# Kernel tuning notes

Hardware: AMD Instinct MI355X
Metric: run time of the kernel (lower is better)

The kernel has to match this reference:

```python
import jax, jax.numpy as jnp
import numpy as np

N_NODES = 100000
HID = 64
IN_DIM = 128


def setup_inputs() -> dict:
    key = jax.random.key(0)
    ks = jax.random.split(key, 12)
    x = jax.random.normal(ks[0], (N_NODES, IN_DIM), dtype=jnp.float32)
    edge_index = jax.random.randint(ks[1], (2, 1600000), 0, N_NODES, dtype=jnp.int64)
    batch = jnp.zeros((N_NODES,), dtype=jnp.int64)
    def glorot(k, shape):
        fan_in, fan_out = shape
        lim = (6.0 / (fan_in + fan_out)) ** 0.5
        return jax.random.uniform(k, shape, jnp.float32, -lim, lim)
    return {
        "x": x,
        "edge_index": edge_index,
        "batch": batch,
        "W1": glorot(ks[2], (IN_DIM, HID)), "b1": jnp.zeros((HID,), jnp.float32),
        "W2": glorot(ks[3], (HID, HID)),   "b2": jnp.zeros((HID,), jnp.float32),
        "W3": glorot(ks[4], (HID, HID)),   "b3": jnp.zeros((HID,), jnp.float32),
        "Wp1": glorot(ks[5], (HID, HID // 2)), "bp1": jnp.zeros((HID // 2,), jnp.float32),
        "Wp2": glorot(ks[6], (HID // 2, 1)),   "bp2": jnp.zeros((1,), jnp.float32),
    }


def _gcn_norm(edge_index, n_nodes):
    # Add self-loops, compute symmetric normalization deg^{-1/2}[src]*deg^{-1/2}[dst]
    loops = jnp.arange(n_nodes, dtype=edge_index.dtype)
    src = jnp.concatenate([edge_index[0], loops])
    dst = jnp.concatenate([edge_index[1], loops])
    deg = jax.ops.segment_sum(jnp.ones_like(dst, dtype=jnp.float32), dst,
                              num_segments=n_nodes)
    dinv = jnp.where(deg > 0, jax.lax.rsqrt(deg), 0.0)
    norm = dinv[src] * dinv[dst]  # [E + N]
    return src, dst, norm


def _gcn_layer(x, src, dst, norm, W, b, n_nodes):
    h = x @ W                       # [N, out]  dense transform first (PyG order)
    msg = h[src] * norm[:, None]    # gather + scale, [E+N, out]
    agg = jax.ops.segment_sum(msg, dst, num_segments=n_nodes)  # scatter-add
    return agg + b


def reference(x, edge_index, batch, W1, b1, W2, b2, W3, b3, Wp1, bp1, Wp2, bp2):
    n = x.shape[0]
    src, dst, norm = _gcn_norm(edge_index, n)
    # eval mode: dropout is identity
    h = jax.nn.relu(_gcn_layer(x, src, dst, norm, W1, b1, n))
    h = jax.nn.relu(_gcn_layer(h, src, dst, norm, W2, b2, n))
    h = jax.nn.relu(_gcn_layer(h, src, dst, norm, W3, b3, n))
    h = jax.nn.relu(h @ Wp1 + bp1)
    return h @ Wp2 + bp2  # [N, 1] node predictions
```

## Files before the change

### kernel.cpp

```cpp
#include <hip/hip_runtime.h>
#include <hip/hip_bf16.h>
#include <hip/hip_fp16.h>

#define NDIM_IN 128
#define HID 64

#define BINW 128
#define NB   782
#define NC   256
#define CAP  3072

typedef _Float16 f16x8 __attribute__((ext_vector_type(8)));
typedef float f32x4 __attribute__((ext_vector_type(4)));

__global__ __launch_bounds__(256) void hist_k(const int* __restrict__ dst,
                                              int* __restrict__ histT, int E) {
  __shared__ int h[NB];
  for (int i = threadIdx.x; i < NB; i += 256) h[i] = 0;
  __syncthreads();
  int E4 = E >> 2;
  int chunk = (E4 + NC - 1) / NC;
  int beg = blockIdx.x * chunk;
  int end = min(E4, beg + chunk);
  const int4* __restrict__ d4 = (const int4*)dst;
  for (int i = beg + (int)threadIdx.x; i < end; i += 256) {
    int4 d = d4[i];
    atomicAdd(&h[d.x >> 7], 1);
    atomicAdd(&h[d.y >> 7], 1);
    atomicAdd(&h[d.z >> 7], 1);
    atomicAdd(&h[d.w >> 7], 1);
  }
  __syncthreads();
  for (int i = threadIdx.x; i < NB; i += 256)
    histT[i * NC + blockIdx.x] = h[i];
}

__global__ __launch_bounds__(256) void scan1(int* __restrict__ g,
                                             int* __restrict__ bs, int len) {
  __shared__ int s[256];
  int t = threadIdx.x;
  int i = blockIdx.x * 256 + t;
  int v = (i < len) ? g[i] : 0;
  s[t] = v;
  __syncthreads();
  for (int off = 1; off < 256; off <<= 1) {
    int x = (t >= off) ? s[t - off] : 0;
    __syncthreads();
    s[t] += x;
    __syncthreads();
  }
  if (i < len) g[i] = s[t] - v;
  if (t == 255) bs[blockIdx.x] = s[255];
}

__global__ __launch_bounds__(1024) void scan2(int* __restrict__ bs, int nb) {
  __shared__ int s[1024];
  int t = threadIdx.x;
  int v = (t < nb) ? bs[t] : 0;
  s[t] = v;
  __syncthreads();
  for (int off = 1; off < 1024; off <<= 1) {
    int x = (t >= off) ? s[t - off] : 0;
    __syncthreads();
    s[t] += x;
    __syncthreads();
  }
  if (t < nb) bs[t] = s[t] - v;
}

__global__ __launch_bounds__(256) void scatter_k(const int* __restrict__ src,
                                                 const int* __restrict__ dst,
                                                 const int* __restrict__ S,
                                                 const int* __restrict__ bsum,
                                                 int* __restrict__ tmp, int E) {
  __shared__ int cur[NB];
  for (int i = threadIdx.x; i < NB; i += 256)
    cur[i] = S[i * NC + blockIdx.x] + bsum[i];
  __syncthreads();
  int E4 = E >> 2;
  int chunk = (E4 + NC - 1) / NC;
  int beg = blockIdx.x * chunk;
  int end = min(E4, beg + chunk);
  const int4* __restrict__ d4 = (const int4*)dst;
  const int4* __restrict__ s4 = (const int4*)src;
  for (int i = beg + (int)threadIdx.x; i < end; i += 256) {
    int4 d = d4[i];
    int4 sv = s4[i];
    int p0 = atomicAdd(&cur[d.x >> 7], 1); tmp[p0] = (sv.x << 7) | (d.x & 127);
    int p1 = atomicAdd(&cur[d.y >> 7], 1); tmp[p1] = (sv.y << 7) | (d.y & 127);
    int p2 = atomicAdd(&cur[d.z >> 7], 1); tmp[p2] = (sv.z << 7) | (d.z & 127);
    int p3 = atomicAdd(&cur[d.w >> 7], 1); tmp[p3] = (sv.w << 7) | (d.w & 127);
  }
}

__global__ __launch_bounds__(256) void binsort_k(const int* __restrict__ tmp,
                                                 const int* __restrict__ bsum,
                                                 int* __restrict__ col,
                                                 int* __restrict__ rp,
                                                 float* __restrict__ dinv,
                                                 int n, int E) {
  int bin = blockIdx.x;
  int base = bsum[bin];
  int end = (bin == NB - 1) ? E : bsum[bin + 1];
  int m = end - base;
  __shared__ int cnt[BINW];
  __shared__ int offs[BINW];
  __shared__ int cur[BINW];
  __shared__ int buf[CAP];
  int t = threadIdx.x;
  if (t < BINW) cnt[t] = 0;
  __syncthreads();
  for (int i = t; i < m; i += 256) {
    int p = tmp[base + i];
    atomicAdd(&cnt[p & (BINW - 1)], 1);
  }
  __syncthreads();
  if (t < BINW) offs[t] = cnt[t];
  __syncthreads();
  for (int off = 1; off < BINW; off <<= 1) {
    int x = (t < BINW && t >= off) ? offs[t - off] : 0;
    __syncthreads();
    if (t < BINW) offs[t] += x;
    __syncthreads();
  }
  if (t < BINW) {
    int ex = offs[t] - cnt[t];
    cur[t] = ex;
    int v = bin * BINW + t;
    if (v < n) {
      rp[v] = base + ex;
      dinv[v] = rsqrtf((float)cnt[t] + 1.0f);
    }
  }
  if (bin == NB - 1 && t == 0) rp[n] = E;
  __syncthreads();
  for (int i = t; i < m; i += 256) {
    int p = tmp[base + i];
    int r = atomicAdd(&cur[p & (BINW - 1)], 1);
    if (r < CAP) buf[r] = p >> 7;
  }
  __syncthreads();
  int mm = min(m, CAP);
  for (int i = t; i < mm; i += 256) col[base + i] = buf[i];
}

template <int K>
__global__ __launch_bounds__(256) void gemm_mfma(const float* __restrict__ X,
                                                 const float* __restrict__ W,
                                                 const float* __restrict__ dinv,
                                                 __half* __restrict__ T,
                                                 int n, int ntiles) {
  constexpr int NCH = K / 32;
  __shared__ float Ds[4][16 * 68];
  int wv = threadIdx.x >> 6;
  int lane = threadIdx.x & 63;
  int colx = lane & 15;
  int quad = lane >> 4;

  f16x8 bf[4][NCH];
#pragma unroll
  for (int t = 0; t < 4; t++)
#pragma unroll
    for (int c = 0; c < NCH; c++) {
      f16x8 b;
#pragma unroll
      for (int j = 0; j < 8; j++)
        b[j] = (_Float16)W[(32 * c + quad * 8 + j) * 64 + 16 * t + colx];
      bf[t][c] = b;
    }

  for (int tile = blockIdx.x * 4 + wv; tile < ntiles; tile += gridDim.x * 4) {
    int node0 = tile * 16;
    f32x4 acc[4] = {{0.f, 0.f, 0.f, 0.f}, {0.f, 0.f, 0.f, 0.f},
                    {0.f, 0.f, 0.f, 0.f}, {0.f, 0.f, 0.f, 0.f}};
    int arow = min(node0 + colx, n - 1);
    const float* __restrict__ xr = X + (size_t)arow * K;
#pragma unroll
    for (int c = 0; c < NCH; c++) {
      float4 x0 = *(const float4*)(xr + 32 * c + quad * 8);
      float4 x1 = *(const float4*)(xr + 32 * c + quad * 8 + 4);
      f16x8 a;
      a[0] = (_Float16)x0.x; a[1] = (_Float16)x0.y;
      a[2] = (_Float16)x0.z; a[3] = (_Float16)x0.w;
      a[4] = (_Float16)x1.x; a[5] = (_Float16)x1.y;
      a[6] = (_Float16)x1.z; a[7] = (_Float16)x1.w;
#pragma unroll
      for (int t = 0; t < 4; t++)
        acc[t] = __builtin_amdgcn_mfma_f32_16x16x32_f16(a, bf[t][c], acc[t], 0, 0, 0);
    }
    float dv[4];
#pragma unroll
    for (int r = 0; r < 4; r++) {
      int nd = min(node0 + quad * 4 + r, n - 1);
      dv[r] = dinv[nd];
    }
#pragma unroll
    for (int t = 0; t < 4; t++)
#pragma unroll
      for (int r = 0; r < 4; r++)
        Ds[wv][(quad * 4 + r) * 68 + 16 * t + colx] = acc[t][r] * dv[r];
    int nd = node0 + colx;
    const float* __restrict__ row = &Ds[wv][colx * 68 + quad * 16];
    float4 y0 = *(const float4*)(row + 0);
    float4 y1 = *(const float4*)(row + 4);
    float4 y2 = *(const float4*)(row + 8);
    float4 y3 = *(const float4*)(row + 12);
    f16x8 o0, o1;
    o0[0] = (_Float16)y0.x; o0[1] = (_Float16)y0.y;
    o0[2] = (_Float16)y0.z; o0[3] = (_Float16)y0.w;
    o0[4] = (_Float16)y1.x; o0[5] = (_Float16)y1.y;
    o0[6] = (_Float16)y1.z; o0[7] = (_Float16)y1.w;
    o1[0] = (_Float16)y2.x; o1[1] = (_Float16)y2.y;
    o1[2] = (_Float16)y2.z; o1[3] = (_Float16)y2.w;
    o1[4] = (_Float16)y3.x; o1[5] = (_Float16)y3.y;
    o1[6] = (_Float16)y3.z; o1[7] = (_Float16)y3.w;
    if (nd < n) {
      uint4* __restrict__ o = (uint4*)(T + (size_t)nd * 64 + quad * 16);
      o[0] = *(uint4*)&o0;
      o[1] = *(uint4*)&o1;
    }
  }
}

__global__ __launch_bounds__(256) void spmm_relu(const int* __restrict__ rp,
                                                 const int* __restrict__ col,
                                                 const __half* __restrict__ T,
                                                 const float* __restrict__ dinv,
                                                 const float* __restrict__ bias,
                                                 float* __restrict__ H, int n) {
  int gid = blockIdx.x * 256 + threadIdx.x;
  int v = gid >> 6;
  int lane = gid & 63;
  if (v >= n) return;
  int g = lane >> 3;
  int sub = lane & 7;
  const uint4* __restrict__ T8 = (const uint4*)T;
  int beg = rp[v], end = rp[v + 1];

  float a0[8], a1[8];
#pragma unroll
  for (int j = 0; j < 8; j++) { a0[j] = 0.f; a1[j] = 0.f; }

  if (g == 0) {
    uint4 w = T8[v * 8 + sub];
    const __half2* h = (const __half2*)&w;
#pragma unroll
    for (int j = 0; j < 4; j++) {
      float2 f = __half22float2(h[j]);
      a0[2 * j] += f.x; a0[2 * j + 1] += f.y;
    }
  }
  int efull = beg + ((end - beg) & ~15);
  for (int e = beg; e < efull; e += 16) {
    int s0 = col[e + g];
    int s1 = col[e + 8 + g];
    uint4 w0 = T8[s0 * 8 + sub];
    uint4 w1 = T8[s1 * 8 + sub];
    const __half2* h0 = (const __half2*)&w0;
    const __half2* h1 = (const __half2*)&w1;
#pragma unroll
    for (int j = 0; j < 4; j++) {
      float2 f0 = __half22float2(h0[j]);
      float2 f1 = __half22float2(h1[j]);
      a0[2 * j] += f0.x; a0[2 * j + 1] += f0.y;
      a1[2 * j] += f1.x; a1[2 * j + 1] += f1.y;
    }
  }
  {
    int i0 = efull + g, i1 = efull + 8 + g;
    if (i0 < end) {
      uint4 w = T8[col[i0] * 8 + sub];
      const __half2* h = (const __half2*)&w;
#pragma unroll
      for (int j = 0; j < 4; j++) {
        float2 f = __half22float2(h[j]);
        a0[2 * j] += f.x; a0[2 * j + 1] += f.y;
      }
    }
    if (i1 < end) {
      uint4 w = T8[col[i1] * 8 + sub];
      const __half2* h = (const __half2*)&w;
#pragma unroll
      for (int j = 0; j < 4; j++) {
        float2 f = __half22float2(h[j]);
        a1[2 * j] += f.x; a1[2 * j + 1] += f.y;
      }
    }
  }
  float s[8];
#pragma unroll
  for (int j = 0; j < 8; j++) s[j] = a0[j] + a1[j];
#pragma unroll
  for (int j = 0; j < 8; j++) s[j] += __shfl_xor(s[j], 8);
#pragma unroll
  for (int j = 0; j < 8; j++) s[j] += __shfl_xor(s[j], 16);
#pragma unroll
  for (int j = 0; j < 8; j++) s[j] += __shfl_xor(s[j], 32);
  if (lane < 8) {
    float di = dinv[v];
    const float4* __restrict__ b4 = (const float4*)bias;
    float4 bA = b4[sub * 2], bB = b4[sub * 2 + 1];
    float4 rA, rB;
    rA.x = di * s[0] + bA.x; rA.y = di * s[1] + bA.y;
    rA.z = di * s[2] + bA.z; rA.w = di * s[3] + bA.w;
    rB.x = di * s[4] + bB.x; rB.y = di * s[5] + bB.y;
    rB.z = di * s[6] + bB.z; rB.w = di * s[7] + bB.w;
    rA.x = rA.x > 0.f ? rA.x : 0.f;  rA.y = rA.y > 0.f ? rA.y : 0.f;
    rA.z = rA.z > 0.f ? rA.z : 0.f;  rA.w = rA.w > 0.f ? rA.w : 0.f;
    rB.x = rB.x > 0.f ? rB.x : 0.f;  rB.y = rB.y > 0.f ? rB.y : 0.f;
    rB.z = rB.z > 0.f ? rB.z : 0.f;  rB.w = rB.w > 0.f ? rB.w : 0.f;
    float4* __restrict__ o = (float4*)(H + (size_t)v * HID + sub * 8);
    o[0] = rA;
    o[1] = rB;
  }
}

__global__ __launch_bounds__(256) void mlp_head(const float* __restrict__ H,
                                                const float* __restrict__ Wp1,
                                                const float* __restrict__ bp1,
                                                const float* __restrict__ Wp2,
                                                const float* __restrict__ bp2,
                                                float* __restrict__ out, int n) {
  __shared__ float W1t[32 * 64];
  __shared__ float w2s[32];
  __shared__ float b1s[32];
  for (int i = threadIdx.x; i < 64 * 32; i += 256) {
    int k = i >> 5, j = i & 31;
    W1t[j * 64 + k] = Wp1[i];
  }
  if (threadIdx.x < 32) {
    w2s[threadIdx.x] = Wp2[threadIdx.x];
    b1s[threadIdx.x] = bp1[threadIdx.x];
  }
  __syncthreads();
  int node = blockIdx.x * 256 + threadIdx.x;
  if (node >= n) return;
  float4 h[16];
  const float4* __restrict__ hr = (const float4*)(H + (size_t)node * 64);
#pragma unroll
  for (int j = 0; j < 16; j++) h[j] = hr[j];
  float o = bp2[0];
#pragma unroll
  for (int j = 0; j < 32; j++) {
    const float4* wr = (const float4*)(W1t + j * 64);
    float4 a4 = make_float4(0.f, 0.f, 0.f, 0.f);
#pragma unroll
    for (int k = 0; k < 16; k++) {
      float4 w = wr[k];
      a4.x += h[k].x * w.x;
      a4.y += h[k].y * w.y;
      a4.z += h[k].z * w.z;
      a4.w += h[k].w * w.w;
    }
    float a = a4.x + a4.y + a4.z + a4.w + b1s[j];
    a = a > 0.f ? a : 0.f;
    o += a * w2s[j];
  }
  out[node] = o;
}

extern "C" void kernel_launch(void* const* d_in, const int* in_sizes, int n_in,
                              void* d_out, int out_size, void* d_ws, size_t ws_size,
                              hipStream_t stream) {
  const float* x   = (const float*)d_in[0];
  const int* edge  = (const int*)d_in[1];
  const float* W1  = (const float*)d_in[3];
  const float* b1  = (const float*)d_in[4];
  const float* W2  = (const float*)d_in[5];
  const float* b2  = (const float*)d_in[6];
  const float* W3  = (const float*)d_in[7];
  const float* b3  = (const float*)d_in[8];
  const float* Wp1 = (const float*)d_in[9];
  const float* bp1 = (const float*)d_in[10];
  const float* Wp2 = (const float*)d_in[11];
  const float* bp2 = (const float*)d_in[12];
  float* out = (float*)d_out;

  const int n = in_sizes[0] / NDIM_IN;
  const int E = in_sizes[1] / 2;
  const int* src = edge;
  const int* dst = edge + E;

  char* ws = (char*)d_ws;
  size_t off = 0;
  auto carve = [&](size_t bytes) {
    char* p = ws + off;
    off = (off + bytes + 255) & ~(size_t)255;
    return p;
  };
  int*    histT = (int*)carve((size_t)NB * NC * 4);
  int*    bsum  = (int*)carve(1024 * 4);
  int*    tmp   = (int*)carve((size_t)E * 4);
  int*    col   = (int*)carve((size_t)E * 4);
  int*    rp    = (int*)carve(((size_t)n + 1) * 4);
  float*  dinv  = (float*)carve((size_t)n * 4);
  __half* bufT  = (__half*)carve((size_t)n * HID * 2);
  float*  bufA  = (float*)carve((size_t)n * HID * 4);
  (void)ws_size; (void)n_in; (void)out_size;

  const int nbN = (n + 255) / 256;
  const int ntiles = (n + 15) >> 4;
  const int nbM = 782;
  const int scan_len = NB * NC;
  const int nbScan = (scan_len + 255) / 256;

  hist_k<<<NC, 256, 0, stream>>>(dst, histT, E);
  scan1<<<nbScan, 256, 0, stream>>>(histT, bsum, scan_len);
  scan2<<<1, 1024, 0, stream>>>(bsum, nbScan);
  scatter_k<<<NC, 256, 0, stream>>>(src, dst, histT, bsum, tmp, E);
  binsort_k<<<NB, 256, 0, stream>>>(tmp, bsum, col, rp, dinv, n, E);

  const int nbSp = ((n * 64) + 255) / 256;

  gemm_mfma<128><<<nbM, 256, 0, stream>>>(x, W1, dinv, bufT, n, ntiles);
  spmm_relu<<<nbSp, 256, 0, stream>>>(rp, col, bufT, dinv, b1, bufA, n);
  gemm_mfma<64><<<nbM, 256, 0, stream>>>(bufA, W2, dinv, bufT, n, ntiles);
  spmm_relu<<<nbSp, 256, 0, stream>>>(rp, col, bufT, dinv, b2, bufA, n);
  gemm_mfma<64><<<nbM, 256, 0, stream>>>(bufA, W3, dinv, bufT, n, ntiles);
  spmm_relu<<<nbSp, 256, 0, stream>>>(rp, col, bufT, dinv, b3, bufA, n);
  mlp_head<<<nbN, 256, 0, stream>>>(bufA, Wp1, bp1, Wp2, bp2, out, n);
}
```

Before: 226.4 us.

## Map one 8-lane group per node in SpMM instead of one wavefront per node

The SpMM kernel previously assigned a full 64-lane wavefront to each node, splitting the node's edges across 8 lane groups and combining them with cross-lane shuffle reductions, with only 8 lanes storing. Now each 8-lane group owns a node and walks all of that node's edges sequentially, unrolled by two. This removes the shuffle reductions and the idle lanes for low-degree nodes, and launches eight times fewer blocks. The trade-off is less memory-level parallelism per node and load imbalance within a wavefront when degrees vary, since the eight nodes in a wave have different edge counts.

After: 205.0 us. 9.5% less time.

```diff
diff --git a/kernel.cpp b/kernel.cpp
--- a/kernel.cpp
+++ b/kernel.cpp
@@ -228,34 +228,34 @@
                                                  const float* __restrict__ dinv,
                                                  const float* __restrict__ bias,
                                                  float* __restrict__ H, int n) {
-  int gid = blockIdx.x * 256 + threadIdx.x;
-  int v = gid >> 6;
-  int lane = gid & 63;
-  if (v >= n) return;
+  int lane = threadIdx.x & 63;
+  int wv = threadIdx.x >> 6;
   int g = lane >> 3;
   int sub = lane & 7;
+  int v = blockIdx.x * 32 + wv * 8 + g;
+  bool valid = v < n;
+  if (!valid) v = n - 1;
   const uint4* __restrict__ T8 = (const uint4*)T;
-  int beg = rp[v], end = rp[v + 1];
+  int beg = rp[v];
+  int end = rp[v + 1];
 
   float a0[8], a1[8];
-#pragma unroll
-  for (int j = 0; j < 8; j++) { a0[j] = 0.f; a1[j] = 0.f; }
-
-  if (g == 0) {
-    uint4 w = T8[v * 8 + sub];
+  {
+    uint4 w = T8[(size_t)v * 8 + sub];
     const __half2* h = (const __half2*)&w;
 #pragma unroll
     for (int j = 0; j < 4; j++) {
       float2 f = __half22float2(h[j]);
-      a0[2 * j] += f.x; a0[2 * j + 1] += f.y;
-    }
-  }
-  int efull = beg + ((end - beg) & ~15);
-  for (int e = beg; e < efull; e += 16) {
-    int s0 = col[e + g];
-    int s1 = col[e + 8 + g];
-    uint4 w0 = T8[s0 * 8 + sub];
-    uint4 w1 = T8[s1 * 8 + sub];
+      a0[2 * j] = f.x; a0[2 * j + 1] = f.y;
+      a1[2 * j] = 0.f; a1[2 * j + 1] = 0.f;
+    }
+  }
+  int e = beg;
+  for (; e + 2 <= end; e += 2) {
+    int s0 = col[e];
+    int s1 = col[e + 1];
+    uint4 w0 = T8[(size_t)s0 * 8 + sub];
+    uint4 w1 = T8[(size_t)s1 * 8 + sub];
     const __half2* h0 = (const __half2*)&w0;
     const __half2* h1 = (const __half2*)&w1;
 #pragma unroll
@@ -266,49 +266,33 @@
       a1[2 * j] += f1.x; a1[2 * j + 1] += f1.y;
     }
   }
-  {
-    int i0 = efull + g, i1 = efull + 8 + g;
-    if (i0 < end) {
-      uint4 w = T8[col[i0] * 8 + sub];
-      const __half2* h = (const __half2*)&w;
-#pragma unroll
-      for (int j = 0; j < 4; j++) {
-        float2 f = __half22float2(h[j]);
-        a0[2 * j] += f.x; a0[2 * j + 1] += f.y;
-      }
-    }
-    if (i1 < end) {
-      uint4 w = T8[col[i1] * 8 + sub];
-      const __half2* h = (const __half2*)&w;
-#pragma unroll
-      for (int j = 0; j < 4; j++) {
-        float2 f = __half22float2(h[j]);
-        a1[2 * j] += f.x; a1[2 * j + 1] += f.y;
-      }
-    }
-  }
-  float s[8];
-#pragma unroll
-  for (int j = 0; j < 8; j++) s[j] = a0[j] + a1[j];
-#pragma unroll
-  for (int j = 0; j < 8; j++) s[j] += __shfl_xor(s[j], 8);
-#pragma unroll
-  for (int j = 0; j < 8; j++) s[j] += __shfl_xor(s[j], 16);
-#pragma unroll
-  for (int j = 0; j < 8; j++) s[j] += __shfl_xor(s[j], 32);
-  if (lane < 8) {
-    float di = dinv[v];
-    const float4* __restrict__ b4 = (const float4*)bias;
-    float4 bA = b4[sub * 2], bB = b4[sub * 2 + 1];
-    float4 rA, rB;
-    rA.x = di * s[0] + bA.x; rA.y = di * s[1] + bA.y;
-    rA.z = di * s[2] + bA.z; rA.w = di * s[3] + bA.w;
-    rB.x = di * s[4] + bB.x; rB.y = di * s[5] + bB.y;
-    rB.z = di * s[6] + bB.z; rB.w = di * s[7] + bB.w;
-    rA.x = rA.x > 0.f ? rA.x : 0.f;  rA.y = rA.y > 0.f ? rA.y : 0.f;
-    rA.z = rA.z > 0.f ? rA.z : 0.f;  rA.w = rA.w > 0.f ? rA.w : 0.f;
-    rB.x = rB.x > 0.f ? rB.x : 0.f;  rB.y = rB.y > 0.f ? rB.y : 0.f;
-    rB.z = rB.z > 0.f ? rB.z : 0.f;  rB.w = rB.w > 0.f ? rB.w : 0.f;
+  if (e < end) {
+    int s0 = col[e];
+    uint4 w0 = T8[(size_t)s0 * 8 + sub];
+    const __half2* h0 = (const __half2*)&w0;
+#pragma unroll
+    for (int j = 0; j < 4; j++) {
+      float2 f0 = __half22float2(h0[j]);
+      a0[2 * j] += f0.x; a0[2 * j + 1] += f0.y;
+    }
+  }
+  float di = dinv[v];
+  const float4* __restrict__ b4 = (const float4*)bias;
+  float4 bA = b4[sub * 2], bB = b4[sub * 2 + 1];
+  float4 rA, rB;
+  rA.x = di * (a0[0] + a1[0]) + bA.x;
+  rA.y = di * (a0[1] + a1[1]) + bA.y;
+  rA.z = di * (a0[2] + a1[2]) + bA.z;
+  rA.w = di * (a0[3] + a1[3]) + bA.w;
+  rB.x = di * (a0[4] + a1[4]) + bB.x;
+  rB.y = di * (a0[5] + a1[5]) + bB.y;
+  rB.z = di * (a0[6] + a1[6]) + bB.z;
+  rB.w = di * (a0[7] + a1[7]) + bB.w;
+  rA.x = rA.x > 0.f ? rA.x : 0.f;  rA.y = rA.y > 0.f ? rA.y : 0.f;
+  rA.z = rA.z > 0.f ? rA.z : 0.f;  rA.w = rA.w > 0.f ? rA.w : 0.f;
+  rB.x = rB.x > 0.f ? rB.x : 0.f;  rB.y = rB.y > 0.f ? rB.y : 0.f;
+  rB.z = rB.z > 0.f ? rB.z : 0.f;  rB.w = rB.w > 0.f ? rB.w : 0.f;
+  if (valid) {
     float4* __restrict__ o = (float4*)(H + (size_t)v * HID + sub * 8);
     o[0] = rA;
     o[1] = rB;
@@ -410,7 +394,7 @@
   scatter_k<<<NC, 256, 0, stream>>>(src, dst, histT, bsum, tmp, E);
   binsort_k<<<NB, 256, 0, stream>>>(tmp, bsum, col, rp, dinv, n, E);
 
-  const int nbSp = ((n * 64) + 255) / 256;
+  const int nbSp = (n + 31) / 32;
 
   gemm_mfma<128><<<nbM, 256, 0, stream>>>(x, W1, dinv, bufT, n, ntiles);
   spmm_relu<<<nbSp, 256, 0, stream>>>(rp, col, bufT, dinv, b1, bufA, n);
```
